# Optimization experiments

Measured on AMD Instinct MI355X. Metric: run time of the kernel, lower is better.

Reference implementation:

```python
import jax, jax.numpy as jnp
import numpy as np

# Module constants (match init_kwargs)
G = 8        # number of channel groups (len(list_input_dim))
D = 16       # per-group input dim
L = 1024     # sequence length
B = 16       # batch
E = 8        # num_experts
OUT = 64     # out_channels
KS = 3       # emb_kernel_size
K = 4        # hardcoded self.k in Channel_Embedding
LOSS_COEF = 0.01


def setup_inputs() -> dict:
    key = jax.random.key(0)
    k0, k1, k2, k3 = jax.random.split(key, 4)
    x = jax.random.normal(k0, (B, G * D, L), jnp.float32)
    # torch inits w_gate to zeros (degenerate); use small random weights for meaningful routing
    w_gate = jax.random.normal(k1, (G, D * 5, E), jnp.float32) * 0.1
    conv1_w = jax.random.normal(k2, (G, OUT, D, KS), jnp.float32) * (1.0 / np.sqrt(D * KS))
    conv1_b = jnp.zeros((G, OUT), jnp.float32)
    conv2_w = jax.random.normal(k3, (G, OUT * E, OUT, 1), jnp.float32) * (1.0 / np.sqrt(OUT))
    conv2_b = jnp.zeros((G, OUT * E), jnp.float32)
    return dict(x=x, w_gate=w_gate, conv1_w=conv1_w, conv1_b=conv1_b,
                conv2_w=conv2_w, conv2_b=conv2_b)


def _cv_squared(v):
    # torch: x.float().var() (unbiased) / (mean^2 + eps)
    v = v.astype(jnp.float32)
    return jnp.var(v, ddof=1) / (jnp.mean(v) ** 2 + 1e-10)


def _conv1d(x, w, b):
    # x [B,C,L], w [O,I,K] -> [B,O,L'] (VALID, stride 1)
    y = jax.lax.conv_general_dilated(x, w, (1,), 'VALID',
                                     dimension_numbers=('NCH', 'OIH', 'NCH'))
    return y + b[None, :, None]


def _group_forward(xg, wg, c1w, c1b, c2w, c2b):
    # xg: [B, D, L] single channel group
    Bb = xg.shape[0]
    # gating input: last timesteps [-6:-1] -> [B, D*5]
    gate_in = xg[:, :, -6:-1].reshape(Bb, -1)
    logits = jax.nn.softmax(gate_in @ wg, axis=1)           # [B, E]
    top_v, top_i = jax.lax.top_k(logits, min(K + 1, E))     # [B, K+1]
    tkv, tki = top_v[:, :K], top_i[:, :K]
    gk = tkv / (tkv.sum(1, keepdims=True) + 1e-6)
    gates = jnp.zeros_like(logits).at[jnp.arange(Bb)[:, None], tki].set(gk)  # [B, E]
    load = (gates > 0).sum(0)                               # eval path: _gates_to_load
    loss = _cv_squared(gates.sum(0)) + _cv_squared(load)
    # experts: conv(D->OUT, k=KS) -> tanh -> conv(OUT -> OUT*E, k=1)
    h = jnp.tanh(_conv1d(xg, c1w, c1b))
    raw = _conv1d(h, c2w, c2b)                              # [B, OUT*E, L']
    Lp = raw.shape[-1]
    # channel index = d*E + e (matches torch permute+reshape(B,-1,OUT,E))
    moe = jnp.einsum('bdel,be->bdl', raw.reshape(Bb, OUT, E, Lp), gates)  # [B, OUT, L']
    return moe, loss, gates


def reference(x, w_gate, conv1_w, conv1_b, conv2_w, conv2_b):
    # split channels into G groups of D: [G, B, D, L]
    xg = x.reshape(x.shape[0], G, D, x.shape[-1]).transpose(1, 0, 2, 3)
    moe, loss, gates = jax.vmap(_group_forward)(xg, w_gate, conv1_w, conv1_b, conv2_w, conv2_b)
    combine_features = moe.transpose(1, 0, 2, 3)   # [B, G, OUT, L']
    out_loss = LOSS_COEF * loss.sum()
    gates_out = gates.transpose(1, 2, 0)           # [B, E, G]
    return combine_features, out_loss, gates_out
```

## Files before the change

kernel.cpp:

```cpp
#include <hip/hip_runtime.h>
#include <hip/hip_bf16.h>

#define NG   8
#define ND   16
#define NL   1024
#define NB   16
#define NE   8
#define NOUT 64
#define NKS  3
#define NK   4
#define NLP  1022

#define OUT_LOSS  (NB*NG*NOUT*NLP)
#define OUT_GATES (OUT_LOSS + 1)

__device__ __forceinline__ float tanh_fast(float x) {
    float e = exp2f(x * 2.885390081777927f);
    return 1.0f - 2.0f / (e + 1.0f);
}

__device__ __forceinline__ void compute_gates_f(
    const float* __restrict__ x, const float* __restrict__ wg,
    int g, int b, float gates[8])
{
    float gi[80];
    const float* xrow = x + (size_t)(b * 128 + g * 16) * 1024 + (1024 - 6);
    #pragma unroll
    for (int d = 0; d < 16; ++d) {
        #pragma unroll
        for (int tt = 0; tt < 5; ++tt) gi[d * 5 + tt] = xrow[d * 1024 + tt];
    }

    float lg[8];
    #pragma unroll
    for (int e = 0; e < 8; ++e) lg[e] = 0.f;
    const float* wgg = wg + g * 640;
    #pragma unroll
    for (int j = 0; j < 80; ++j) {
        const float v = gi[j];
        #pragma unroll
        for (int e = 0; e < 8; ++e) lg[e] = fmaf(v, wgg[j * 8 + e], lg[e]);
    }

    float mx = lg[0];
    #pragma unroll
    for (int e = 1; e < 8; ++e) mx = fmaxf(mx, lg[e]);
    float s = 0.f;
    #pragma unroll
    for (int e = 0; e < 8; ++e) { lg[e] = expf(lg[e] - mx); s += lg[e]; }
    const float invsm = 1.f / s;
    #pragma unroll
    for (int e = 0; e < 8; ++e) lg[e] *= invsm;

    int used = 0;
    float tv[4]; int ti[4];
    #pragma unroll
    for (int k = 0; k < 4; ++k) {
        float bv = -1.f; int be = 0;
        #pragma unroll
        for (int e = 0; e < 8; ++e) {
            if (!((used >> e) & 1) && lg[e] > bv) { bv = lg[e]; be = e; }
        }
        tv[k] = bv; ti[k] = be; used |= (1 << be);
    }
    const float s4 = tv[0] + tv[1] + tv[2] + tv[3];
    const float invs = 1.f / (s4 + 1e-6f);
    #pragma unroll
    for (int e = 0; e < 8; ++e) {
        float v = 0.f;
        #pragma unroll
        for (int k = 0; k < 4; ++k) if (ti[k] == e) v = tv[k] * invs;
        gates[e] = v;
    }
}

__global__ __launch_bounds__(256) void prep_kernel(
    const float* __restrict__ x,   const float* __restrict__ wg,
    const float* __restrict__ c1w, const float* __restrict__ c2w,
    const float* __restrict__ c2b,
    float* __restrict__ out, float* __restrict__ weff,
    float* __restrict__ beff, float* __restrict__ w1r)
{
    const int bid = blockIdx.x;
    const int t   = threadIdx.x;

    __shared__ float glds[128][8];
    __shared__ float impa[64], loda[64];
    __shared__ float lossg[8];

    if (bid < 128) {
        const int gb = bid, g = gb >> 4, b = gb & 15;
        float gt[8];
        compute_gates_f(x, wg, g, b, gt);

        const int o  = t >> 2;
        const int iq = (t & 3) * 16;
        const float* w2g = c2w + (size_t)g * 512 * 64 + (size_t)o * 8 * 64 + iq;
        float acc[16];
        #pragma unroll
        for (int q = 0; q < 16; ++q) acc[q] = 0.f;
        #pragma unroll
        for (int e = 0; e < 8; ++e) {
            const float4* src = (const float4*)(w2g + e * 64);
            #pragma unroll
            for (int q = 0; q < 4; ++q) {
                float4 v = src[q];
                acc[q*4+0] = fmaf(gt[e], v.x, acc[q*4+0]);
                acc[q*4+1] = fmaf(gt[e], v.y, acc[q*4+1]);
                acc[q*4+2] = fmaf(gt[e], v.z, acc[q*4+2]);
                acc[q*4+3] = fmaf(gt[e], v.w, acc[q*4+3]);
            }
        }
        float4* dst = (float4*)(weff + (size_t)gb * 4096 + o * 64 + iq);
        #pragma unroll
        for (int q = 0; q < 4; ++q) {
            float4 v; v.x = acc[q*4+0]; v.y = acc[q*4+1];
                      v.z = acc[q*4+2]; v.w = acc[q*4+3];
            dst[q] = v;
        }
        if (t < 64) {
            const float* b2g = c2b + g * 512;
            float a = 0.f;
            #pragma unroll
            for (int e = 0; e < 8; ++e) a = fmaf(gt[e], b2g[t * 8 + e], a);
            beff[gb * 64 + t] = a;
        }
    } else if (bid < 136) {
        const int g = bid - 128;
        for (int idx = t; idx < 48 * 64; idx += 256) {
            const int j = idx >> 6, o = idx & 63;
            w1r[(size_t)(g * 48 + j) * 64 + o] = c1w[(size_t)g * 3072 + o * 48 + j];
        }
    } else {
        float gates[8];
        const int g = t >> 4, b = t & 15;
        if (t < 128) {
            compute_gates_f(x, wg, g, b, gates);
            #pragma unroll
            for (int e = 0; e < 8; ++e) {
                glds[t][e] = gates[e];
                out[OUT_GATES + (b * 8 + e) * 8 + g] = gates[e];
            }
        }
        __syncthreads();
        if (t < 64) {
            const int gg = t >> 3, e = t & 7;
            float si = 0.f, sl = 0.f;
            for (int bb = 0; bb < 16; ++bb) {
                const float v = glds[gg * 16 + bb][e];
                si += v;
                sl += (v > 0.f) ? 1.f : 0.f;
            }
            impa[t] = si; loda[t] = sl;
        }
        __syncthreads();
        if (t < 8) {
            float m1 = 0.f, m2 = 0.f;
            #pragma unroll
            for (int e = 0; e < 8; ++e) { m1 += impa[t * 8 + e]; m2 += loda[t * 8 + e]; }
            m1 *= 0.125f; m2 *= 0.125f;
            float v1 = 0.f, v2 = 0.f;
            #pragma unroll
            for (int e = 0; e < 8; ++e) {
                const float d1 = impa[t * 8 + e] - m1, d2 = loda[t * 8 + e] - m2;
                v1 += d1 * d1; v2 += d2 * d2;
            }
            v1 *= (1.f / 7.f); v2 *= (1.f / 7.f);
            lossg[t] = v1 / (m1 * m1 + 1e-10f) + v2 / (m2 * m2 + 1e-10f);
        }
        __syncthreads();
        if (t == 0) {
            float tot = 0.f;
            #pragma unroll
            for (int gg = 0; gg < 8; ++gg) tot += lossg[gg];
            out[OUT_LOSS] = 0.01f * tot;
        }
    }
}

__global__ __launch_bounds__(256, 4) void main_kernel(
    const float* __restrict__ x,    const float* __restrict__ w1r,
    const float* __restrict__ b1,   const float* __restrict__ weff,
    const float* __restrict__ beff, float* __restrict__ out)
{
    __shared__ float hT[64][128];

    const int bid   = blockIdx.x;
    const int xcd   = bid & 7;
    const int j     = bid >> 3;
    const int gb    = ((j & 15) << 3) | xcd;
    const int tile  = j >> 4;
    const int g     = gb >> 4, b = gb & 15;
    const int t     = threadIdx.x;
    const int lane  = t & 63;
    const int obase = __builtin_amdgcn_readfirstlane((t >> 6) << 4);
    const int c0    = lane * 2;
    const int l0    = tile * 128 + c0;
    const int lc    = (l0 <= NLP - 2) ? l0 : (NLP - 2);

    float a0[16], a1[16];
    const float* b1g = b1 + g * 64 + obase;
    #pragma unroll
    for (int o = 0; o < 16; ++o) { a0[o] = b1g[o]; a1[o] = a0[o]; }

    const float* xb  = x + (size_t)(b * 128 + g * 16) * 1024 + lc;
    const float* wrg = w1r + (size_t)(g * 48) * 64 + obase;

    float2 xaA[8], xcA[8];
    #pragma unroll
    for (int i = 0; i < 8; ++i) {
        xaA[i] = *(const float2*)(xb + i * 1024);
        xcA[i] = *(const float2*)(xb + i * 1024 + 2);
    }
    float2 xaB[8], xcB[8];
    #pragma unroll
    for (int i = 0; i < 8; ++i) {
        xaB[i] = *(const float2*)(xb + (8 + i) * 1024);
        xcB[i] = *(const float2*)(xb + (8 + i) * 1024 + 2);
    }

    #pragma unroll
    for (int i = 0; i < 8; ++i) {
        const float* wr = wrg + i * 192;
        #pragma unroll
        for (int o = 0; o < 16; ++o) {
            const float w0 = wr[o], w1 = wr[64 + o], w2 = wr[128 + o];
            a0[o] = fmaf(w0, xaA[i].x, a0[o]);
            a0[o] = fmaf(w1, xaA[i].y, a0[o]);
            a0[o] = fmaf(w2, xcA[i].x, a0[o]);
            a1[o] = fmaf(w0, xaA[i].y, a1[o]);
            a1[o] = fmaf(w1, xcA[i].x, a1[o]);
            a1[o] = fmaf(w2, xcA[i].y, a1[o]);
        }
    }
    #pragma unroll
    for (int i = 0; i < 8; ++i) {
        const float* wr = wrg + (8 + i) * 192;
        #pragma unroll
        for (int o = 0; o < 16; ++o) {
            const float w0 = wr[o], w1 = wr[64 + o], w2 = wr[128 + o];
            a0[o] = fmaf(w0, xaB[i].x, a0[o]);
            a0[o] = fmaf(w1, xaB[i].y, a0[o]);
            a0[o] = fmaf(w2, xcB[i].x, a0[o]);
            a1[o] = fmaf(w0, xaB[i].y, a1[o]);
            a1[o] = fmaf(w1, xcB[i].x, a1[o]);
            a1[o] = fmaf(w2, xcB[i].y, a1[o]);
        }
    }
    #pragma unroll
    for (int o = 0; o < 16; ++o) {
        float2 hv; hv.x = tanh_fast(a0[o]); hv.y = tanh_fast(a1[o]);
        *(float2*)&hT[obase + o][c0] = hv;
    }

    __syncthreads();

    const float* bef = beff + gb * 64 + obase;
    #pragma unroll
    for (int o = 0; o < 16; ++o) { a0[o] = bef[o]; a1[o] = a0[o]; }

    const float* wef = weff + (size_t)gb * 4096 + (size_t)obase * 64;

    float2 hhA[16], hhB[16];
    #pragma unroll
    for (int i = 0; i < 16; ++i) hhA[i] = *(const float2*)&hT[i][c0];
    #pragma unroll
    for (int i = 0; i < 16; ++i) hhB[i] = *(const float2*)&hT[16 + i][c0];

    #pragma unroll
    for (int o = 0; o < 16; ++o) {
        const float* wr = wef + o * 64;
        #pragma unroll
        for (int i = 0; i < 16; ++i) {
            a0[o] = fmaf(wr[i], hhA[i].x, a0[o]);
            a1[o] = fmaf(wr[i], hhA[i].y, a1[o]);
        }
    }
    #pragma unroll
    for (int i = 0; i < 16; ++i) hhA[i] = *(const float2*)&hT[32 + i][c0];

    #pragma unroll
    for (int o = 0; o < 16; ++o) {
        const float* wr = wef + o * 64 + 16;
        #pragma unroll
        for (int i = 0; i < 16; ++i) {
            a0[o] = fmaf(wr[i], hhB[i].x, a0[o]);
            a1[o] = fmaf(wr[i], hhB[i].y, a1[o]);
        }
    }
    #pragma unroll
    for (int i = 0; i < 16; ++i) hhB[i] = *(const float2*)&hT[48 + i][c0];

    #pragma unroll
    for (int o = 0; o < 16; ++o) {
        const float* wr = wef + o * 64 + 32;
        #pragma unroll
        for (int i = 0; i < 16; ++i) {
            a0[o] = fmaf(wr[i], hhA[i].x, a0[o]);
            a1[o] = fmaf(wr[i], hhA[i].y, a1[o]);
        }
    }
    #pragma unroll
    for (int o = 0; o < 16; ++o) {
        const float* wr = wef + o * 64 + 48;
        #pragma unroll
        for (int i = 0; i < 16; ++i) {
            a0[o] = fmaf(wr[i], hhB[i].x, a0[o]);
            a1[o] = fmaf(wr[i], hhB[i].y, a1[o]);
        }
    }

    if (l0 <= NLP - 2) {
        float* ob = out + ((size_t)((b * 8 + g) * 64 + obase)) * NLP + l0;
        #pragma unroll
        for (int o = 0; o < 16; ++o) {
            float2 v; v.x = a0[o]; v.y = a1[o];
            *(float2*)(ob + (size_t)o * NLP) = v;
        }
    }
}

extern "C" void kernel_launch(void* const* d_in, const int* in_sizes, int n_in,
                              void* d_out, int out_size, void* d_ws, size_t ws_size,
                              hipStream_t stream) {
    const float* x   = (const float*)d_in[0];
    const float* wg  = (const float*)d_in[1];
    const float* c1w = (const float*)d_in[2];
    const float* c1b = (const float*)d_in[3];
    const float* c2w = (const float*)d_in[4];
    const float* c2b = (const float*)d_in[5];
    float* out = (float*)d_out;

    float* ws   = (float*)d_ws;
    float* beff = ws;
    float* weff = ws + 8192;
    float* w1r  = ws + 8192 + 524288;

    prep_kernel<<<137, 256, 0, stream>>>(x, wg, c1w, c2w, c2b, out, weff, beff, w1r);
    main_kernel<<<1024, 256, 0, stream>>>(x, w1r, c1b, weff, beff, out);
}
```

Measured before the change: 125.7 us.

## Compute second expert conv with split-bf16 MFMA instead of scalar FP32 FMAs

The 64x64 gated 1x1 conv is moved from per-thread FP32 FMA loops onto 16x16x32 bf16 MFMA instructions. To keep near-FP32 accuracy, each operand is split into a high bf16 and a residual bf16, and three cross-products are accumulated. The prep kernel now writes the effective weights pre-packed into MFMA fragment layout, and the hidden activations are staged in LDS as fragments rather than as a float tile. The MFMA result layout leaves output stores with a per-row pattern that is less coalesced, and the split-bf16 trick adds packing work and a small accuracy risk.

Result: faster. 116.5 us (-7.3%).

```diff
diff --git a/kernel.cpp b/kernel.cpp
--- a/kernel.cpp
+++ b/kernel.cpp
@@ -14,9 +14,20 @@
 #define OUT_LOSS  (NB*NG*NOUT*NLP)
 #define OUT_GATES (OUT_LOSS + 1)
 
+typedef short bf16x8 __attribute__((ext_vector_type(8)));
+typedef float f32x4  __attribute__((ext_vector_type(4)));
+
 __device__ __forceinline__ float tanh_fast(float x) {
     float e = exp2f(x * 2.885390081777927f);
     return 1.0f - 2.0f / (e + 1.0f);
+}
+
+__device__ __forceinline__ unsigned fbits(float a) { return __builtin_bit_cast(unsigned, a); }
+__device__ __forceinline__ float resid(float a) {
+    return a - __builtin_bit_cast(float, fbits(a) & 0xFFFF0000u);
+}
+__device__ __forceinline__ int pack2(float a, float b) {
+    return (int)((fbits(a) >> 16) | (fbits(b) & 0xFFFF0000u));
 }
 
 __device__ __forceinline__ void compute_gates_f(
@@ -30,7 +41,6 @@
         #pragma unroll
         for (int tt = 0; tt < 5; ++tt) gi[d * 5 + tt] = xrow[d * 1024 + tt];
     }
-
     float lg[8];
     #pragma unroll
     for (int e = 0; e < 8; ++e) lg[e] = 0.f;
@@ -41,7 +51,6 @@
         #pragma unroll
         for (int e = 0; e < 8; ++e) lg[e] = fmaf(v, wgg[j * 8 + e], lg[e]);
     }
-
     float mx = lg[0];
     #pragma unroll
     for (int e = 1; e < 8; ++e) mx = fmaxf(mx, lg[e]);
@@ -78,7 +87,7 @@
     const float* __restrict__ x,   const float* __restrict__ wg,
     const float* __restrict__ c1w, const float* __restrict__ c2w,
     const float* __restrict__ c2b,
-    float* __restrict__ out, float* __restrict__ weff,
+    float* __restrict__ out, int4* __restrict__ weffA,
     float* __restrict__ beff, float* __restrict__ w1r)
 {
     const int bid = blockIdx.x;
@@ -111,12 +120,24 @@
                 acc[q*4+3] = fmaf(gt[e], v.w, acc[q*4+3]);
             }
         }
-        float4* dst = (float4*)(weff + (size_t)gb * 4096 + o * 64 + iq);
-        #pragma unroll
-        for (int q = 0; q < 4; ++q) {
-            float4 v; v.x = acc[q*4+0]; v.y = acc[q*4+1];
-                      v.z = acc[q*4+2]; v.w = acc[q*4+3];
-            dst[q] = v;
+        const int mt  = o >> 4;
+        const int ks  = iq >> 5;
+        const int lgA = (iq & 31) >> 3;
+        int4* wdst = weffA + gb * 1024 + mt * 128 + ks * 64;
+        #pragma unroll
+        for (int R = 0; R < 2; ++R) {
+            int4 whi, wlo;
+            whi.x = pack2(acc[R*8+0], acc[R*8+1]);
+            whi.y = pack2(acc[R*8+2], acc[R*8+3]);
+            whi.z = pack2(acc[R*8+4], acc[R*8+5]);
+            whi.w = pack2(acc[R*8+6], acc[R*8+7]);
+            wlo.x = pack2(resid(acc[R*8+0]), resid(acc[R*8+1]));
+            wlo.y = pack2(resid(acc[R*8+2]), resid(acc[R*8+3]));
+            wlo.z = pack2(resid(acc[R*8+4]), resid(acc[R*8+5]));
+            wlo.w = pack2(resid(acc[R*8+6]), resid(acc[R*8+7]));
+            const int slot = (lgA + R) * 16 + (o & 15);
+            wdst[slot]       = whi;
+            wdst[512 + slot] = wlo;
         }
         if (t < 64) {
             const float* b2g = c2b + g * 512;
@@ -180,20 +201,21 @@
 
 __global__ __launch_bounds__(256, 4) void main_kernel(
     const float* __restrict__ x,    const float* __restrict__ w1r,
-    const float* __restrict__ b1,   const float* __restrict__ weff,
+    const float* __restrict__ b1,   const int4* __restrict__ weffA,
     const float* __restrict__ beff, float* __restrict__ out)
 {
-    __shared__ float hT[64][128];
+    __shared__ int4 hfrag[2048];
 
     const int bid   = blockIdx.x;
     const int xcd   = bid & 7;
-    const int j     = bid >> 3;
-    const int gb    = ((j & 15) << 3) | xcd;
-    const int tile  = j >> 4;
+    const int jj    = bid >> 3;
+    const int gb    = ((jj & 15) << 3) | xcd;
+    const int tile  = jj >> 4;
     const int g     = gb >> 4, b = gb & 15;
     const int t     = threadIdx.x;
     const int lane  = t & 63;
-    const int obase = __builtin_amdgcn_readfirstlane((t >> 6) << 4);
+    const int wv    = t >> 6;
+    const int obase = __builtin_amdgcn_readfirstlane(wv << 4);
     const int c0    = lane * 2;
     const int l0    = tile * 128 + c0;
     const int lc    = (l0 <= NLP - 2) ? l0 : (NLP - 2);
@@ -218,7 +240,6 @@
         xaB[i] = *(const float2*)(xb + (8 + i) * 1024);
         xcB[i] = *(const float2*)(xb + (8 + i) * 1024 + 2);
     }
-
     #pragma unroll
     for (int i = 0; i < 8; ++i) {
         const float* wr = wrg + i * 192;
@@ -248,74 +269,86 @@
         }
     }
     #pragma unroll
-    for (int o = 0; o < 16; ++o) {
-        float2 hv; hv.x = tanh_fast(a0[o]); hv.y = tanh_fast(a1[o]);
-        *(float2*)&hT[obase + o][c0] = hv;
-    }
+    for (int o = 0; o < 16; ++o) { a0[o] = tanh_fast(a0[o]); a1[o] = tanh_fast(a1[o]); }
+
+    {
+        const int ks1 = obase >> 5;
+        const int lg0 = (obase >> 3) & 3;
+        #pragma unroll
+        for (int cp = 0; cp < 2; ++cp) {
+            const int c = c0 + cp;
+            const int ub = (c >> 4) * 64 + lg0 * 16 + (c & 15);
+            #pragma unroll
+            for (int R = 0; R < 2; ++R) {
+                float h0, h1, h2, h3, h4, h5, h6, h7;
+                if (cp == 0) {
+                    h0=a0[R*8+0]; h1=a0[R*8+1]; h2=a0[R*8+2]; h3=a0[R*8+3];
+                    h4=a0[R*8+4]; h5=a0[R*8+5]; h6=a0[R*8+6]; h7=a0[R*8+7];
+                } else {
+                    h0=a1[R*8+0]; h1=a1[R*8+1]; h2=a1[R*8+2]; h3=a1[R*8+3];
+                    h4=a1[R*8+4]; h5=a1[R*8+5]; h6=a1[R*8+6]; h7=a1[R*8+7];
+                }
+                int4 whi, wlo;
+                whi.x = pack2(h0, h1); whi.y = pack2(h2, h3);
+                whi.z = pack2(h4, h5); whi.w = pack2(h6, h7);
+                wlo.x = pack2(resid(h0), resid(h1)); wlo.y = pack2(resid(h2), resid(h3));
+                wlo.z = pack2(resid(h4), resid(h5)); wlo.w = pack2(resid(h6), resid(h7));
+                hfrag[ks1 * 512 + ub + R * 16]       = whi;
+                hfrag[(2 + ks1) * 512 + ub + R * 16] = wlo;
+            }
+        }
+    }
+
+    const int rbase = (lane >> 4) << 2;
+    const float* befp = beff + gb * 64 + rbase;
+    f32x4 bias0 = *(const f32x4*)(befp);
+    f32x4 bias1 = *(const f32x4*)(befp + 16);
+    f32x4 bias2 = *(const f32x4*)(befp + 32);
+    f32x4 bias3 = *(const f32x4*)(befp + 48);
 
     __syncthreads();
 
-    const float* bef = beff + gb * 64 + obase;
-    #pragma unroll
-    for (int o = 0; o < 16; ++o) { a0[o] = bef[o]; a1[o] = a0[o]; }
-
-    const float* wef = weff + (size_t)gb * 4096 + (size_t)obase * 64;
-
-    float2 hhA[16], hhB[16];
-    #pragma unroll
-    for (int i = 0; i < 16; ++i) hhA[i] = *(const float2*)&hT[i][c0];
-    #pragma unroll
-    for (int i = 0; i < 16; ++i) hhB[i] = *(const float2*)&hT[16 + i][c0];
-
-    #pragma unroll
-    for (int o = 0; o < 16; ++o) {
-        const float* wr = wef + o * 64;
-        #pragma unroll
-        for (int i = 0; i < 16; ++i) {
-            a0[o] = fmaf(wr[i], hhA[i].x, a0[o]);
-            a1[o] = fmaf(wr[i], hhA[i].y, a1[o]);
-        }
-    }
-    #pragma unroll
-    for (int i = 0; i < 16; ++i) hhA[i] = *(const float2*)&hT[32 + i][c0];
-
-    #pragma unroll
-    for (int o = 0; o < 16; ++o) {
-        const float* wr = wef + o * 64 + 16;
-        #pragma unroll
-        for (int i = 0; i < 16; ++i) {
-            a0[o] = fmaf(wr[i], hhB[i].x, a0[o]);
-            a1[o] = fmaf(wr[i], hhB[i].y, a1[o]);
-        }
-    }
-    #pragma unroll
-    for (int i = 0; i < 16; ++i) hhB[i] = *(const float2*)&hT[48 + i][c0];
-
-    #pragma unroll
-    for (int o = 0; o < 16; ++o) {
-        const float* wr = wef + o * 64 + 32;
-        #pragma unroll
-        for (int i = 0; i < 16; ++i) {
-            a0[o] = fmaf(wr[i], hhA[i].x, a0[o]);
-            a1[o] = fmaf(wr[i], hhA[i].y, a1[o]);
-        }
-    }
-    #pragma unroll
-    for (int o = 0; o < 16; ++o) {
-        const float* wr = wef + o * 64 + 48;
-        #pragma unroll
-        for (int i = 0; i < 16; ++i) {
-            a0[o] = fmaf(wr[i], hhB[i].x, a0[o]);
-            a1[o] = fmaf(wr[i], hhB[i].y, a1[o]);
-        }
-    }
-
-    if (l0 <= NLP - 2) {
-        float* ob = out + ((size_t)((b * 8 + g) * 64 + obase)) * NLP + l0;
-        #pragma unroll
-        for (int o = 0; o < 16; ++o) {
-            float2 v; v.x = a0[o]; v.y = a1[o];
-            *(float2*)(ob + (size_t)o * NLP) = v;
+    const int nt0 = wv * 2;
+    f32x4 acc[4][2];
+    acc[0][0] = bias0; acc[0][1] = bias0;
+    acc[1][0] = bias1; acc[1][1] = bias1;
+    acc[2][0] = bias2; acc[2][1] = bias2;
+    acc[3][0] = bias3; acc[3][1] = bias3;
+
+    const int4* wAbase = weffA + gb * 1024 + lane;
+    #pragma unroll
+    for (int ks = 0; ks < 2; ++ks) {
+        bf16x8 Bh0 = *(const bf16x8*)&hfrag[ks * 512 + nt0 * 64 + lane];
+        bf16x8 Bh1 = *(const bf16x8*)&hfrag[ks * 512 + (nt0 + 1) * 64 + lane];
+        bf16x8 Bl0 = *(const bf16x8*)&hfrag[(2 + ks) * 512 + nt0 * 64 + lane];
+        bf16x8 Bl1 = *(const bf16x8*)&hfrag[(2 + ks) * 512 + (nt0 + 1) * 64 + lane];
+        #pragma unroll
+        for (int mt = 0; mt < 4; ++mt) {
+            bf16x8 Ah = *(const bf16x8*)(wAbase + mt * 128 + ks * 64);
+            bf16x8 Al = *(const bf16x8*)(wAbase + 512 + mt * 128 + ks * 64);
+            acc[mt][0] = __builtin_amdgcn_mfma_f32_16x16x32_bf16(Ah, Bh0, acc[mt][0], 0, 0, 0);
+            acc[mt][1] = __builtin_amdgcn_mfma_f32_16x16x32_bf16(Ah, Bh1, acc[mt][1], 0, 0, 0);
+            acc[mt][0] = __builtin_amdgcn_mfma_f32_16x16x32_bf16(Ah, Bl0, acc[mt][0], 0, 0, 0);
+            acc[mt][1] = __builtin_amdgcn_mfma_f32_16x16x32_bf16(Ah, Bl1, acc[mt][1], 0, 0, 0);
+            acc[mt][0] = __builtin_amdgcn_mfma_f32_16x16x32_bf16(Al, Bh0, acc[mt][0], 0, 0, 0);
+            acc[mt][1] = __builtin_amdgcn_mfma_f32_16x16x32_bf16(Al, Bh1, acc[mt][1], 0, 0, 0);
+        }
+    }
+
+    const int colg = tile * 128 + nt0 * 16 + (lane & 15);
+    float* outg = out + (size_t)((b * 8 + g) * 64) * NLP;
+    #pragma unroll
+    for (int mt = 0; mt < 4; ++mt) {
+        #pragma unroll
+        for (int j = 0; j < 2; ++j) {
+            const int cg = colg + j * 16;
+            if (cg < NLP) {
+                float* orow = outg + (size_t)(mt * 16 + rbase) * NLP + cg;
+                orow[0]             = acc[mt][j][0];
+                orow[(size_t)NLP]   = acc[mt][j][1];
+                orow[(size_t)NLP*2] = acc[mt][j][2];
+                orow[(size_t)NLP*3] = acc[mt][j][3];
+            }
         }
     }
 }
@@ -331,11 +364,11 @@
     const float* c2b = (const float*)d_in[5];
     float* out = (float*)d_out;
 
-    float* ws   = (float*)d_ws;
-    float* beff = ws;
-    float* weff = ws + 8192;
-    float* w1r  = ws + 8192 + 524288;
-
-    prep_kernel<<<137, 256, 0, stream>>>(x, wg, c1w, c2w, c2b, out, weff, beff, w1r);
-    main_kernel<<<1024, 256, 0, stream>>>(x, w1r, c1b, weff, beff, out);
-}
+    char* ws    = (char*)d_ws;
+    int4* weffA = (int4*)ws;
+    float* beff = (float*)(ws + (size_t)131072*16);
+    float* w1r  = beff + 8192;
+
+    prep_kernel<<<137, 256, 0, stream>>>(x, wg, c1w, c2w, c2b, out, weffA, beff, w1r);
+    main_kernel<<<1024, 256, 0, stream>>>(x, w1r, c1b, weffA, beff, out);
+}
```
